# Optimization experiments

Measured on AMD Instinct MI355X. Metric: run time of the kernel, lower is better.

## Reference

```python
import jax, jax.numpy as jnp
import numpy as np
from jax import lax

B, J, I = 32, 48, 48          # batch, target len, source len
W = 2                          # target_window_size
CTX = 2 * W + 1                # 5
E, H = 128, 256                # embedding_size, hidden_units
VT, VS = 32000, 32000          # target / source vocab
S = 2 * J                      # HMM states (word + null)


def setup_inputs() -> dict:
    key = jax.random.key(0)
    ks = jax.random.split(key, 12)
    inp = {
        "target_embedding": jax.random.normal(ks[0], (VT, E), jnp.float32) * 0.02,
        "W_bridge": jax.random.normal(ks[1], (E * CTX, E), jnp.float32) * 0.02,
        "W_hidden": jax.random.normal(ks[2], (E, H), jnp.float32) * 0.02,
        "b_hidden": jnp.zeros((H,), jnp.float32),
        "W_vocab": jax.random.normal(ks[3], (H, VS), jnp.float32) * 0.02,
        "b_vocab": jnp.zeros((VS,), jnp.float32),
        "transition": jax.random.uniform(ks[4], (B, S, S), jnp.float32, 0.01, 1.0),
        "initial_transition": jax.random.uniform(ks[5], (B, S), jnp.float32, 0.01, 1.0),
        "targets_ctx": jax.random.randint(ks[6], (B, J * CTX), 0, VT, jnp.int32),
        "targets_ctx_null": jax.random.randint(ks[7], (B, J * CTX), 0, VT, jnp.int32),
        "sources": jax.random.randint(ks[8], (B, I), 0, VS, jnp.int32),
    }
    return inp


def _emission(emb, Wb, Wh, bh, Wv, bv, ctx_ids, sources):
    # embedding lookup + context reshape: [B, J*CTX, E] -> [B, J, CTX*E]
    x = emb[ctx_ids].reshape(ctx_ids.shape[0], -1, CTX * E)
    h = jnp.tanh(jnp.einsum('bjc,ce,eh->bjh', x, Wb, Wh) + bh)  # bridge+hidden
    probs = jax.nn.softmax(h @ Wv + bv, axis=-1)                # [B, J, VS]
    # per-example gather of source token columns -> [B, J, I]
    return jax.vmap(lambda p, s: p[:, s])(probs, sources)


def _forward_backward(pi, A, em):
    # pi [B,S], A [B,S,S], em [B,S,I]; scaled HMM forward-backward
    e = jnp.moveaxis(em, 2, 0)  # [I, B, S]
    a0 = pi * e[0]
    c0 = a0.sum(-1, keepdims=True)
    a0 = a0 / c0

    def fstep(a, ei):
        an = jnp.einsum('bs,bst->bt', a, A) * ei
        c = an.sum(-1, keepdims=True)
        an = an / c
        return an, (an, c)

    _, (alphas, cs) = lax.scan(fstep, a0, e[1:])
    alphas = jnp.concatenate([a0[None], alphas], 0)          # [I,B,S]
    cs = jnp.concatenate([c0[None], cs], 0)                  # [I,B,1]

    def bstep(b, inp):
        ei, ci = inp
        bn = jnp.einsum('bst,bt->bs', A, ei * b) / ci
        return bn, bn

    bI = jnp.ones_like(a0)
    _, betas_rev = lax.scan(bstep, bI, (e[1:][::-1], cs[1:][::-1]))
    betas = jnp.concatenate([betas_rev[::-1], bI[None]], 0)  # [I,B,S]

    gamma = alphas * betas                                   # state posteriors
    loglik = jnp.log(cs[..., 0]).sum(0)                      # [B]
    return jnp.moveaxis(gamma, 0, 2), loglik


def reference(target_embedding, W_bridge, W_hidden, b_hidden, W_vocab, b_vocab,
              transition, initial_transition, targets_ctx, targets_ctx_null, sources):
    em_word = _emission(target_embedding, W_bridge, W_hidden, b_hidden,
                        W_vocab, b_vocab, targets_ctx, sources)       # [B,J,I]
    em_null = _emission(target_embedding, W_bridge, W_hidden, b_hidden,
                        W_vocab, b_vocab, targets_ctx_null, sources)  # [B,J,I]
    emission = jnp.concatenate([em_word, em_null], axis=1)            # [B,2J,I]
    gamma, loglik = _forward_backward(initial_transition, transition, emission)
    return gamma, -loglik
```

## Files before the change

kernel.cpp:

```cpp
#include <hip/hip_runtime.h>
#include <hip/hip_bf16.h>

#define NB 32
#define NJ 48
#define NI 48
#define NCTX 5
#define NE 128
#define NH 256
#define NVS 32000
#define NS 96
#define NR 3072

typedef __attribute__((ext_vector_type(8))) short bf16x8;
typedef __attribute__((ext_vector_type(4))) float f32x4;

__device__ __forceinline__ unsigned short f2b(float f) {
  __hip_bfloat16 h = __float2bfloat16(f);
  return *reinterpret_cast<unsigned short*>(&h);
}
__device__ __forceinline__ float wave_sum(float v) {
  v += __shfl_xor(v, 1);
  v += __shfl_xor(v, 2);
  v += __shfl_xor(v, 4);
  v += __shfl_xor(v, 8);
  v += __shfl_xor(v, 16);
  v += __shfl_xor(v, 32);
  return v;
}
__device__ __forceinline__ void gload_lds16(const void* g, void* l) {
  __builtin_amdgcn_global_load_lds(
      (const __attribute__((address_space(1))) void*)g,
      (__attribute__((address_space(3))) void*)l, 16, 0, 0);
}

__global__ __launch_bounds__(256) void k_transpose(const float* __restrict__ Wv,
                                                   unsigned char* __restrict__ Wv8) {
  __shared__ float tile[64][65];
  int t = threadIdx.x;
  int v0 = blockIdx.x * 64, k0 = blockIdx.y * 64;
  {
    int kr = t >> 4, vq = t & 15;
#pragma unroll
    for (int it = 0; it < 4; ++it) {
      float4 v = *(const float4*)&Wv[(k0 + kr + 16 * it) * NVS + v0 + vq * 4];
      tile[kr + 16 * it][vq * 4 + 0] = v.x;
      tile[kr + 16 * it][vq * 4 + 1] = v.y;
      tile[kr + 16 * it][vq * 4 + 2] = v.z;
      tile[kr + 16 * it][vq * 4 + 3] = v.w;
    }
  }
  __syncthreads();
  {
    int vl = t >> 2, kq = t & 3;
    unsigned int q8[4];
#pragma unroll
    for (int d = 0; d < 4; ++d) {
      float f0 = tile[kq * 16 + d * 4 + 0][vl] * 64.0f;
      float f1 = tile[kq * 16 + d * 4 + 1][vl] * 64.0f;
      float f2 = tile[kq * 16 + d * 4 + 2][vl] * 64.0f;
      float f3 = tile[kq * 16 + d * 4 + 3][vl] * 64.0f;
      int w = __builtin_amdgcn_cvt_pk_fp8_f32(f0, f1, 0, false);
      w = __builtin_amdgcn_cvt_pk_fp8_f32(f2, f3, w, true);
      q8[d] = (unsigned int)w;
    }
    *(uint4*)&Wv8[(v0 + vl) * 256 + k0 + kq * 16] = *(uint4*)q8;
  }
}

__global__ __launch_bounds__(256) void k_t2b(const float* __restrict__ src,
                                             unsigned short* __restrict__ dst,
                                             int R, int C) {
  __shared__ float tile[64][65];
  int t = threadIdx.x;
  int r0 = blockIdx.x * 64, c0 = blockIdx.y * 64;
  {
    int rr = t >> 4, cq = t & 15;
#pragma unroll
    for (int it = 0; it < 4; ++it) {
      float4 v = *(const float4*)&src[(r0 + rr + 16 * it) * C + c0 + cq * 4];
      tile[rr + 16 * it][cq * 4 + 0] = v.x;
      tile[rr + 16 * it][cq * 4 + 1] = v.y;
      tile[rr + 16 * it][cq * 4 + 2] = v.z;
      tile[rr + 16 * it][cq * 4 + 3] = v.w;
    }
  }
  __syncthreads();
  {
    int cc = t >> 2, rq = t & 3;
    unsigned short pk[16];
#pragma unroll
    for (int q = 0; q < 16; ++q) pk[q] = f2b(tile[rq * 16 + q][cc]);
    *(uint4*)&dst[(c0 + cc) * R + r0 + rq * 16] = *(uint4*)&pk[0];
    *(uint4*)&dst[(c0 + cc) * R + r0 + rq * 16 + 8] = *(uint4*)&pk[8];
  }
}

__global__ __launch_bounds__(256) void k_xb(const float* __restrict__ emb,
                                            const unsigned short* __restrict__ Wbt,
                                            const int* __restrict__ tc, const int* __restrict__ tcn,
                                            unsigned short* __restrict__ xb) {
  __shared__ unsigned short Ax[64 * 72];
  __shared__ unsigned short Bw[128 * 72];
  __shared__ unsigned short xout[64 * 136];
  int t = threadIdx.x;
  int r0 = blockIdx.x * 64;
  int wave = t >> 6, lane = t & 63;
  int wm = wave >> 1, wn = wave & 1;
  int lg = lane >> 4, lr = lane & 15;
  int arow = t >> 2, aseg = t & 3;
  int r = r0 + arow;
  int half = r / 1536, rem = r % 1536, bb = rem / 48, jj = rem % 48;
  const int* ids = half ? tcn : tc;
  int brow = t >> 1, bseg = t & 1;

  f32x4 acc[2][4];
#pragma unroll
  for (int m = 0; m < 2; ++m)
#pragma unroll
    for (int n = 0; n < 4; ++n) acc[m][n] = (f32x4){0.f, 0.f, 0.f, 0.f};

  for (int step = 0; step < 10; ++step) {
    int k0 = step * 64;
    int p = k0 >> 7;
    int e0 = k0 & 127;
    {
      int id = ids[bb * 240 + jj * 5 + p];
      const float4* er = (const float4*)&emb[id * 128 + e0 + aseg * 16];
      unsigned short pk[16];
#pragma unroll
      for (int q = 0; q < 4; ++q) {
        float4 v = er[q];
        pk[q * 4 + 0] = f2b(v.x);
        pk[q * 4 + 1] = f2b(v.y);
        pk[q * 4 + 2] = f2b(v.z);
        pk[q * 4 + 3] = f2b(v.w);
      }
      *(uint4*)&Ax[arow * 72 + aseg * 16] = *(uint4*)&pk[0];
      *(uint4*)&Ax[arow * 72 + aseg * 16 + 8] = *(uint4*)&pk[8];
    }
    {
      const uint4* wp = (const uint4*)&Wbt[brow * 640 + k0 + bseg * 32];
      uint4* dp = (uint4*)&Bw[brow * 72 + bseg * 32];
      uint4 w0 = wp[0], w1 = wp[1], w2 = wp[2], w3 = wp[3];
      dp[0] = w0; dp[1] = w1; dp[2] = w2; dp[3] = w3;
    }
    __syncthreads();
#pragma unroll
    for (int kk = 0; kk < 2; ++kk) {
      bf16x8 a[2], b[4];
#pragma unroll
      for (int m = 0; m < 2; ++m)
        a[m] = *(const bf16x8*)&Ax[(wm * 32 + m * 16 + lr) * 72 + kk * 32 + lg * 8];
#pragma unroll
      for (int n = 0; n < 4; ++n)
        b[n] = *(const bf16x8*)&Bw[(wn * 64 + n * 16 + lr) * 72 + kk * 32 + lg * 8];
#pragma unroll
      for (int m = 0; m < 2; ++m)
#pragma unroll
        for (int n = 0; n < 4; ++n)
          acc[m][n] = __builtin_amdgcn_mfma_f32_16x16x32_bf16(a[m], b[n], acc[m][n], 0, 0, 0);
    }
    __syncthreads();
  }
#pragma unroll
  for (int m = 0; m < 2; ++m)
#pragma unroll
    for (int n = 0; n < 4; ++n)
#pragma unroll
      for (int g = 0; g < 4; ++g)
        xout[(wm * 32 + m * 16 + lg * 4 + g) * 136 + wn * 64 + n * 16 + lr] = f2b(acc[m][n][g]);
  __syncthreads();
  {
    int orow = t >> 2, os = t & 3;
#pragma unroll
    for (int i = 0; i < 4; ++i)
      ((uint4*)&xb[(r0 + orow) * 128])[os * 4 + i] = *(uint4*)&xout[orow * 136 + (os * 4 + i) * 8];
  }
}

__global__ __launch_bounds__(256) void k_h(const unsigned short* __restrict__ xb,
                                           const unsigned short* __restrict__ Wht,
                                           const float* __restrict__ bh,
                                           unsigned char* __restrict__ hb8) {
  __shared__ char smem[69632];
  unsigned short* Asm = (unsigned short*)smem;
  unsigned short* Bsm = (unsigned short*)(smem + 34816);
  unsigned char* o8 = (unsigned char*)smem;
  int t = threadIdx.x;
  int r0 = blockIdx.x * 128, n0 = blockIdx.y * 128;
  int wave = t >> 6, lane = t & 63;
  int wm = wave >> 1, wn = wave & 1;
  int lg = lane >> 4, lr = lane & 15;
  {
    int row = t >> 1, seg = t & 1;
#pragma unroll
    for (int i = 0; i < 8; ++i) {
      *(uint4*)&Asm[row * 136 + seg * 64 + i * 8] = *(const uint4*)&xb[(r0 + row) * 128 + seg * 64 + i * 8];
      *(uint4*)&Bsm[row * 136 + seg * 64 + i * 8] = *(const uint4*)&Wht[(n0 + row) * 128 + seg * 64 + i * 8];
    }
  }
  __syncthreads();
  f32x4 acc[4][4];
#pragma unroll
  for (int m = 0; m < 4; ++m)
#pragma unroll
    for (int n = 0; n < 4; ++n) acc[m][n] = (f32x4){0.f, 0.f, 0.f, 0.f};
#pragma unroll
  for (int kk = 0; kk < 4; ++kk) {
    bf16x8 a[4], b[4];
#pragma unroll
    for (int m = 0; m < 4; ++m)
      a[m] = *(const bf16x8*)&Asm[(wm * 64 + m * 16 + lr) * 136 + kk * 32 + lg * 8];
#pragma unroll
    for (int n = 0; n < 4; ++n)
      b[n] = *(const bf16x8*)&Bsm[(wn * 64 + n * 16 + lr) * 136 + kk * 32 + lg * 8];
#pragma unroll
    for (int m = 0; m < 4; ++m)
#pragma unroll
      for (int n = 0; n < 4; ++n)
        acc[m][n] = __builtin_amdgcn_mfma_f32_16x16x32_bf16(a[m], b[n], acc[m][n], 0, 0, 0);
  }
  __syncthreads();
#pragma unroll
  for (int n = 0; n < 4; ++n) {
    int cl = wn * 64 + n * 16 + lr;
    float bvv = bh[n0 + cl];
#pragma unroll
    for (int m = 0; m < 4; ++m) {
#pragma unroll
      for (int g = 0; g < 4; ++g) {
        int rl = wm * 64 + m * 16 + lg * 4 + g;
        float hv = tanhf(acc[m][n][g] + bvv);
        int p8 = __builtin_amdgcn_cvt_pk_fp8_f32(hv * 256.0f, 0.0f, 0, false);
        o8[rl * 144 + cl] = (unsigned char)(p8 & 0xFF);
      }
    }
  }
  __syncthreads();
  {
    int row = t >> 1, seg = t & 1;
#pragma unroll
    for (int i = 0; i < 4; ++i)
      *(uint4*)&hb8[(r0 + row) * 256 + n0 + seg * 64 + i * 16] = *(uint4*)&o8[row * 144 + seg * 64 + i * 16];
  }
}

__global__ __launch_bounds__(256) void k_denom(const unsigned char* __restrict__ hb8,
                                               const unsigned char* __restrict__ Wv8,
                                               const float* __restrict__ bv,
                                               float* __restrict__ dpart) {
  __shared__ unsigned char Asm[128 * 64];
  __shared__ unsigned char Bsm[128 * 64];
  __shared__ float red2[2][128];
  int t = threadIdx.x;
  int bid = blockIdx.x;
  int xcd = bid & 7;
  int pos = bid >> 3;
  int tile = xcd * 750 + pos;
  int vt = tile / 24, rt = tile % 24;
  int v0 = vt * 128, r0 = rt * 128;
  int wave = t >> 6, lane = t & 63;
  int wm = wave >> 1, wn = wave & 1;
  int lg = lane >> 4, lr = lane & 15;
  int srow = lane >> 2;
  int sseg = (lane & 3) ^ (srow & 3);

  f32x4 acc[4][4];
#pragma unroll
  for (int m = 0; m < 4; ++m)
#pragma unroll
    for (int n = 0; n < 4; ++n) acc[m][n] = (f32x4){0.f, 0.f, 0.f, 0.f};

  for (int k0 = 0; k0 < 256; k0 += 64) {
#pragma unroll
    for (int c = 0; c < 2; ++c) {
      int inst = wave * 2 + c;
      int row = inst * 16 + srow;
      gload_lds16(&hb8[(r0 + row) * 256 + k0 + sseg * 16], &Asm[inst * 1024]);
      gload_lds16(&Wv8[(v0 + row) * 256 + k0 + sseg * 16], &Bsm[inst * 1024]);
    }
    __syncthreads();
#pragma unroll
    for (int kk = 0; kk < 2; ++kk) {
      long long a[4], b[4];
#pragma unroll
      for (int m = 0; m < 4; ++m) {
        int rr = wm * 64 + m * 16 + lr;
        int off = rr * 64 + ((((kk << 1) | (lg >> 1)) ^ (rr & 3)) << 4) + ((lg & 1) << 3);
        a[m] = *(const long long*)&Asm[off];
      }
#pragma unroll
      for (int n = 0; n < 4; ++n) {
        int rr = wn * 64 + n * 16 + lr;
        int off = rr * 64 + ((((kk << 1) | (lg >> 1)) ^ (rr & 3)) << 4) + ((lg & 1) << 3);
        b[n] = *(const long long*)&Bsm[off];
      }
#pragma unroll
      for (int m = 0; m < 4; ++m)
#pragma unroll
        for (int n = 0; n < 4; ++n)
          acc[m][n] = __builtin_amdgcn_mfma_f32_16x16x32_fp8_fp8(a[m], b[n], acc[m][n], 0, 0, 0);
    }
    __syncthreads();
  }

  const float SC = 6.103515625e-05f;
  float rs[4][4];
#pragma unroll
  for (int m = 0; m < 4; ++m)
#pragma unroll
    for (int g = 0; g < 4; ++g) rs[m][g] = 0.f;
#pragma unroll
  for (int m = 0; m < 4; ++m) {
#pragma unroll
    for (int n = 0; n < 4; ++n) {
      float bvv = bv[v0 + wn * 64 + n * 16 + lr];
#pragma unroll
      for (int g = 0; g < 4; ++g) rs[m][g] += __expf(acc[m][n][g] * SC + bvv);
    }
  }
#pragma unroll
  for (int m = 0; m < 4; ++m)
#pragma unroll
    for (int g = 0; g < 4; ++g) {
      float v = rs[m][g];
      v += __shfl_xor(v, 1);
      v += __shfl_xor(v, 2);
      v += __shfl_xor(v, 4);
      v += __shfl_xor(v, 8);
      rs[m][g] = v;
    }
  if (lr == 0) {
#pragma unroll
    for (int m = 0; m < 4; ++m)
#pragma unroll
      for (int g = 0; g < 4; ++g)
        red2[wn][wm * 64 + m * 16 + lg * 4 + g] = rs[m][g];
  }
  __syncthreads();
  if (t < 128) dpart[vt * NR + r0 + t] = red2[0][t] + red2[1][t];
}

__global__ void k_reduce(const float* __restrict__ dpart, float* __restrict__ dsum) {
  int r = blockIdx.x * 256 + threadIdx.x;
  float s = 0.f;
  for (int vt = 0; vt < 250; ++vt) s += dpart[vt * NR + r];
  dsum[r] = s;
}

__global__ __launch_bounds__(64) void k_emis(const unsigned char* __restrict__ hb8,
                                             const unsigned char* __restrict__ Wv8,
                                             const float* __restrict__ bv,
                                             const float* __restrict__ dsum,
                                             const int* __restrict__ src,
                                             float* __restrict__ em) {
  __shared__ unsigned char A8[48 * 256];
  __shared__ unsigned char B8[48 * 256];
  int t = threadIdx.x;
  int bh = blockIdx.x;
  int b = bh & 31, half = bh >> 5;
  int row4 = t >> 4, seg = t & 15;
  int rbase = half * 1536 + b * 48;
#pragma unroll
  for (int c = 0; c < 12; ++c) {
    int row = c * 4 + row4;
    int gseg = seg ^ (row & 15);
    gload_lds16(&hb8[(rbase + row) * 256 + gseg * 16], &A8[c * 1024]);
    int sv = src[b * 48 + row];
    gload_lds16(&Wv8[sv * 256 + gseg * 16], &B8[c * 1024]);
  }
  __syncthreads();
  int lg = t >> 4, lr = t & 15;
  f32x4 acc[3][3];
#pragma unroll
  for (int m = 0; m < 3; ++m)
#pragma unroll
    for (int n = 0; n < 3; ++n) acc[m][n] = (f32x4){0.f, 0.f, 0.f, 0.f};
#pragma unroll
  for (int kk = 0; kk < 8; ++kk) {
    long long a[3], bb[3];
#pragma unroll
    for (int m = 0; m < 3; ++m) {
      int rr = m * 16 + lr;
      int off = rr * 256 + ((((kk << 1) | (lg >> 1)) ^ (rr & 15)) << 4) + ((lg & 1) << 3);
      a[m] = *(const long long*)&A8[off];
      bb[m] = *(const long long*)&B8[off];
    }
#pragma unroll
    for (int m = 0; m < 3; ++m)
#pragma unroll
      for (int n = 0; n < 3; ++n)
        acc[m][n] = __builtin_amdgcn_mfma_f32_16x16x32_fp8_fp8(a[m], bb[n], acc[m][n], 0, 0, 0);
  }
  const float SC = 6.103515625e-05f;
#pragma unroll
  for (int n = 0; n < 3; ++n) {
    int i = n * 16 + lr;
    int sv = src[b * 48 + i];
    float bvv = bv[sv];
#pragma unroll
    for (int m = 0; m < 3; ++m) {
#pragma unroll
      for (int g = 0; g < 4; ++g) {
        int j = m * 16 + lg * 4 + g;
        float val = __expf(acc[m][n][g] * SC + bvv) / dsum[rbase + j];
        em[b * 4608 + (half * 48 + j) * 48 + i] = val;
      }
    }
  }
}

__global__ __launch_bounds__(192) void k_fb(const float* __restrict__ Atr, const float* __restrict__ pi,
                                            const float* __restrict__ em, float* __restrict__ alph,
                                            float* __restrict__ betas, float* __restrict__ out1) {
  __shared__ float A_st[96 * 97];
  __shared__ float em_lds[48 * 97];
  __shared__ __align__(16) float vec_lds[96];
  __shared__ float red[3];
  int t = threadIdx.x;
  int bid = blockIdx.x;
  int b = bid & 31;
  int role = bid >> 5;
  int col = t >> 1, half = t & 1;
  int base = b * 4608;

  for (int idx = t; idx < 96 * 96; idx += 192) {
    int s = idx / 96, tt = idx % 96;
    A_st[s * 97 + tt] = Atr[b * 9216 + idx];
  }
  for (int idx = t; idx < 96 * 48; idx += 192) {
    int s = idx / 48, i = idx % 48;
    em_lds[i * 97 + s] = em[base + idx];
  }
  __syncthreads();

  float Areg[48];
  if (role == 0) {
#pragma unroll
    for (int ss = 0; ss < 48; ++ss) Areg[ss] = A_st[(half * 48 + ss) * 97 + col];

    float llsum;
    {
      float v = pi[b * 96 + col] * em_lds[0 * 97 + col];
      float ws = half ? 0.f : v;
      ws = wave_sum(ws);
      if ((t & 63) == 0) red[t >> 6] = ws;
      __syncthreads();
      float c = red[0] + red[1] + red[2];
      float a = v / c;
      if (!half) {
        vec_lds[col] = a;
        alph[base + col] = a;
      }
      llsum = logf(c);
      __syncthreads();
    }
    for (int i = 1; i < 48; ++i) {
      float p = 0.f;
      const float4* ap = (const float4*)&vec_lds[half * 48];
#pragma unroll
      for (int q = 0; q < 12; ++q) {
        float4 av = ap[q];
        p += av.x * Areg[4 * q] + av.y * Areg[4 * q + 1] + av.z * Areg[4 * q + 2] + av.w * Areg[4 * q + 3];
      }
      p += __shfl_xor(p, 1);
      float an = p * em_lds[i * 97 + col];
      float ws = half ? 0.f : an;
      ws = wave_sum(ws);
      if ((t & 63) == 0) red[t >> 6] = ws;
      __syncthreads();
      float c = red[0] + red[1] + red[2];
      float a = an / c;
      if (!half) {
        vec_lds[col] = a;
        alph[base + i * 96 + col] = a;
      }
      llsum += logf(c);
      __syncthreads();
    }
    if (t == 0) out1[b] = -llsum;
  } else {
#pragma unroll
    for (int tt = 0; tt < 48; ++tt) Areg[tt] = A_st[col * 97 + half * 48 + tt];

    if (!half) {
      betas[base + 47 * 96 + col] = 1.0f;
      vec_lds[col] = em_lds[47 * 97 + col];
    }
    __syncthreads();
    for (int i = 46; i >= 0; --i) {
      float p = 0.f;
      const float4* ep = (const float4*)&vec_lds[half * 48];
#pragma unroll
      for (int q = 0; q < 12; ++q) {
        float4 ev = ep[q];
        p += ev.x * Areg[4 * q] + ev.y * Areg[4 * q + 1] + ev.z * Areg[4 * q + 2] + ev.w * Areg[4 * q + 3];
      }
      p += __shfl_xor(p, 1);
      float ws = half ? 0.f : p;
      ws = wave_sum(ws);
      if ((t & 63) == 0) red[t >> 6] = ws;
      __syncthreads();
      float c = red[0] + red[1] + red[2];
      float bt = p / c;
      if (!half) {
        betas[base + i * 96 + col] = bt;
        vec_lds[col] = em_lds[i * 97 + col] * bt;
      }
      __syncthreads();
    }
  }
}

__global__ __launch_bounds__(128) void k_gamma(const float* __restrict__ alph,
                                               const float* __restrict__ betas,
                                               float* __restrict__ out0) {
  __shared__ float red[2];
  int b = blockIdx.x, i = blockIdx.y;
  int t = threadIdx.x;
  float g = 0.f;
  if (t < 96) g = alph[b * 4608 + i * 96 + t] * betas[b * 4608 + i * 96 + t];
  float ws = wave_sum(g);
  if ((t & 63) == 0) red[t >> 6] = ws;
  __syncthreads();
  float c = red[0] + red[1];
  if (t < 96) out0[b * 4608 + t * 48 + i] = g / c;
}

extern "C" void kernel_launch(void* const* d_in, const int* in_sizes, int n_in,
                              void* d_out, int out_size, void* d_ws, size_t ws_size,
                              hipStream_t stream) {
  const float* emb = (const float*)d_in[0];
  const float* Wb  = (const float*)d_in[1];
  const float* Wh  = (const float*)d_in[2];
  const float* bh  = (const float*)d_in[3];
  const float* Wv  = (const float*)d_in[4];
  const float* bv  = (const float*)d_in[5];
  const float* Atr = (const float*)d_in[6];
  const float* pi  = (const float*)d_in[7];
  const int* tc    = (const int*)d_in[8];
  const int* tcn   = (const int*)d_in[9];
  const int* src   = (const int*)d_in[10];

  float* out0 = (float*)d_out;
  float* out1 = out0 + NB * NS * NI;

  char* ws = (char*)d_ws;
  unsigned char* wv8 = (unsigned char*)(ws);
  unsigned char* hb8 = (unsigned char*)(ws + 8192000);
  float* dpart       = (float*)(ws + 8978432);
  float* betas       = (float*)(ws + 8978432);
  float* dsum        = (float*)(ws + 12050432);
  float* em          = (float*)(ws + 12062720);
  float* alph        = (float*)(ws + 12652544);
  unsigned short* wbt = (unsigned short*)(ws + 13242368);
  unsigned short* wht = (unsigned short*)(ws + 13406208);
  unsigned short* xb  = (unsigned short*)(ws + 13471744);

  k_transpose<<<dim3(500, 4), 256, 0, stream>>>(Wv, wv8);
  k_t2b<<<dim3(10, 2), 256, 0, stream>>>(Wb, wbt, 640, 128);
  k_t2b<<<dim3(2, 4), 256, 0, stream>>>(Wh, wht, 128, 256);
  k_xb<<<48, 256, 0, stream>>>(emb, wbt, tc, tcn, xb);
  k_h<<<dim3(24, 2), 256, 0, stream>>>(xb, wht, bh, hb8);
  k_denom<<<6000, 256, 0, stream>>>(hb8, wv8, bv, dpart);
  k_reduce<<<12, 256, 0, stream>>>(dpart, dsum);
  k_emis<<<64, 64, 0, stream>>>(hb8, wv8, bv, dsum, src, em);
  k_fb<<<64, 192, 0, stream>>>(Atr, pi, em, alph, betas, out1);
  k_gamma<<<dim3(32, 48), 128, 0, stream>>>(alph, betas, out0);
}
```

Before: 172.1 us.

## Load full K=256 tiles into LDS once in denominator GEMM

The softmax-denominator FP8 GEMM kernel now stages the entire 128x256 A and B tiles into 64KB of shared memory up front, using a 16-way XOR swizzle. It then runs all four K steps without intermediate barriers, replacing the per-64-K load/sync loop. The reduction buffer is aliased onto the same shared memory, with an added barrier before reuse. This removes three barrier round-trips and lets all global loads be in flight at once, but the larger LDS footprint lowers occupancy to about one or two blocks per CU and gives no overlap of loads with MFMA.

```diff
diff --git a/kernel.cpp b/kernel.cpp
--- a/kernel.cpp
+++ b/kernel.cpp
@@ -249,9 +249,10 @@
                                                const unsigned char* __restrict__ Wv8,
                                                const float* __restrict__ bv,
                                                float* __restrict__ dpart) {
-  __shared__ unsigned char Asm[128 * 64];
-  __shared__ unsigned char Bsm[128 * 64];
-  __shared__ float red2[2][128];
+  __shared__ __align__(16) char smem[65536];
+  unsigned char* Asm = (unsigned char*)smem;
+  unsigned char* Bsm = (unsigned char*)(smem + 32768);
+  float* red2 = (float*)smem;
   int t = threadIdx.x;
   int bid = blockIdx.x;
   int xcd = bid & 7;
@@ -262,8 +263,20 @@
   int wave = t >> 6, lane = t & 63;
   int wm = wave >> 1, wn = wave & 1;
   int lg = lane >> 4, lr = lane & 15;
-  int srow = lane >> 2;
-  int sseg = (lane & 3) ^ (srow & 3);
+
+  {
+    int rloc = lane >> 4;
+    int seg = lane & 15;
+#pragma unroll
+    for (int c = 0; c < 8; ++c) {
+      int chunk = wave * 8 + c;
+      int row = chunk * 4 + rloc;
+      int gseg = seg ^ (row & 15);
+      gload_lds16(&hb8[(r0 + row) * 256 + gseg * 16], &Asm[chunk * 1024]);
+      gload_lds16(&Wv8[(v0 + row) * 256 + gseg * 16], &Bsm[chunk * 1024]);
+    }
+  }
+  __syncthreads();
 
   f32x4 acc[4][4];
 #pragma unroll
@@ -271,29 +284,22 @@
 #pragma unroll
     for (int n = 0; n < 4; ++n) acc[m][n] = (f32x4){0.f, 0.f, 0.f, 0.f};
 
-  for (int k0 = 0; k0 < 256; k0 += 64) {
-#pragma unroll
-    for (int c = 0; c < 2; ++c) {
-      int inst = wave * 2 + c;
-      int row = inst * 16 + srow;
-      gload_lds16(&hb8[(r0 + row) * 256 + k0 + sseg * 16], &Asm[inst * 1024]);
-      gload_lds16(&Wv8[(v0 + row) * 256 + k0 + sseg * 16], &Bsm[inst * 1024]);
-    }
-    __syncthreads();
+#pragma unroll
+  for (int K = 0; K < 4; ++K) {
 #pragma unroll
     for (int kk = 0; kk < 2; ++kk) {
+      int lseg = (K << 2) + (kk << 1) + (lg >> 1);
+      int hb = (lg & 1) << 3;
       long long a[4], b[4];
 #pragma unroll
       for (int m = 0; m < 4; ++m) {
         int rr = wm * 64 + m * 16 + lr;
-        int off = rr * 64 + ((((kk << 1) | (lg >> 1)) ^ (rr & 3)) << 4) + ((lg & 1) << 3);
-        a[m] = *(const long long*)&Asm[off];
+        a[m] = *(const long long*)&Asm[rr * 256 + ((lseg ^ lr) << 4) + hb];
       }
 #pragma unroll
       for (int n = 0; n < 4; ++n) {
         int rr = wn * 64 + n * 16 + lr;
-        int off = rr * 64 + ((((kk << 1) | (lg >> 1)) ^ (rr & 3)) << 4) + ((lg & 1) << 3);
-        b[n] = *(const long long*)&Bsm[off];
+        b[n] = *(const long long*)&Bsm[rr * 256 + ((lseg ^ lr) << 4) + hb];
       }
 #pragma unroll
       for (int m = 0; m < 4; ++m)
@@ -301,7 +307,6 @@
         for (int n = 0; n < 4; ++n)
           acc[m][n] = __builtin_amdgcn_mfma_f32_16x16x32_fp8_fp8(a[m], b[n], acc[m][n], 0, 0, 0);
     }
-    __syncthreads();
   }
 
   const float SC = 6.103515625e-05f;
@@ -330,15 +335,16 @@
       v += __shfl_xor(v, 8);
       rs[m][g] = v;
     }
+  __syncthreads();
   if (lr == 0) {
 #pragma unroll
     for (int m = 0; m < 4; ++m)
 #pragma unroll
       for (int g = 0; g < 4; ++g)
-        red2[wn][wm * 64 + m * 16 + lg * 4 + g] = rs[m][g];
-  }
-  __syncthreads();
-  if (t < 128) dpart[vt * NR + r0 + t] = red2[0][t] + red2[1][t];
+        red2[wn * 128 + wm * 64 + m * 16 + lg * 4 + g] = rs[m][g];
+  }
+  __syncthreads();
+  if (t < 128) dpart[vt * NR + r0 + t] = red2[t] + red2[128 + t];
 }
 
 __global__ void k_reduce(const float* __restrict__ dpart, float* __restrict__ dsum) {
```

Result: faster. 161.6 us (-6.1%).
